# Optimization experiments

Measured on AMD Instinct MI355X. Metric: run time of the kernel, lower is better.

## Reference

```python
import jax, jax.numpy as jnp
import numpy as np

M_DIM = 32          # vec_dim m
L1 = L2 = L3 = L4 = 3
L_TOT = L1 * L2 * L3 * L4   # 81
R = 2               # rank1..rank4 window size
B_SZ = 4
D_SZ = 16           # D1 = D2 = D3 = D4


def _make_bbasis():
    # Bbasis[idx, i] = prod_k cos(2*pi*(j_k+1)/(i+2)), idx = flattened (j1,j2,j3,j4)
    i = jnp.arange(M_DIM, dtype=jnp.float32)
    def c(Lk):
        j = jnp.arange(Lk, dtype=jnp.float32)
        return jnp.cos(2.0 * jnp.pi * (j[:, None] + 1.0) / (i[None, :] + 2.0))  # [Lk, m]
    c1, c2, c3, c4 = c(L1), c(L2), c(L3), c(L4)
    Bb = (c1[:, None, None, None, :] * c2[None, :, None, None, :]
          * c3[None, None, :, None, :] * c4[None, None, None, :, :])
    return Bb.reshape(L_TOT, M_DIM)


def _window_basis_idx(n1, n2, n3, n4):
    # linear mode, drop: window top-left coords are 0..n_k-1 with step 1
    j1 = jnp.arange(n1) % L1
    j2 = jnp.arange(n2) % L2
    j3 = jnp.arange(n3) % L3
    j4 = jnp.arange(n4) % L4
    idx = (((j1[:, None, None, None] * L2 + j2[None, :, None, None]) * L3
            + j3[None, None, :, None]) * L4 + j4[None, None, None, :])
    return idx.reshape(-1)  # [n_windows]


def setup_inputs() -> dict:
    key = jax.random.key(0)
    k1, k2, k3 = jax.random.split(key, 3)
    arr_batch = jax.random.normal(k1, (B_SZ, D_SZ, D_SZ, D_SZ, D_SZ, M_DIM), dtype=jnp.float32)
    # M initialized near identity (nn.init.eye_ + perturbation so grads are non-trivial)
    M = jnp.eye(M_DIM, dtype=jnp.float32) + 0.01 * jax.random.normal(k2, (M_DIM, M_DIM), dtype=jnp.float32)
    # Acoeff ~ U(-0.1, 0.1) as in reset_parameters
    Acoeff = jax.random.uniform(k3, (M_DIM, L_TOT), dtype=jnp.float32, minval=-0.1, maxval=0.1)
    Bbasis = _make_bbasis()  # fixed buffer, computed deterministically
    return {"arr_batch": arr_batch, "M": M, "Acoeff": Acoeff, "Bbasis": Bbasis}


def reference(arr_batch, M, Acoeff, Bbasis):
    Bsz, D1, D2, D3, D4, m = arr_batch.shape
    # map every vector through M (x @ M.T); avg-pooling commutes with the linear map,
    # matching `mapped = windows @ M.T` then mean over the window
    mapped = jnp.einsum('bpqrsm,nm->bpqrsn', arr_batch, M)
    # 4D sliding window (rank=2 per dim, stride 1, 'drop' -> VALID), rank_op='avg'
    win = (1, R, R, R, R, 1)
    agg = jax.lax.reduce_window(mapped, 0.0, jax.lax.add, win, (1,) * 6, 'VALID') / float(R ** 4)
    n1, n2, n3, n4 = agg.shape[1:5]
    n_win = n1 * n2 * n3 * n4
    agg = agg.reshape(Bsz, n_win, m)            # [B, W, m]
    idx = _window_basis_idx(n1, n2, n3, n4)     # [W]
    phi = Bbasis[idx]                           # [W, m]
    # t_k = Acoeff[:, j_k] * (Bbasis[j_k, :] . agg_k); representation = mean_k t_k
    s = jnp.einsum('bwm,wm->bw', agg, phi)      # [B, W]
    t = s[:, :, None] * Acoeff.T[idx][None]     # [B, W, m]
    return t.mean(axis=1)                       # [B, m]
```

## Files before the change

kernel.cpp:

```cpp
#include <hip/hip_runtime.h>


static __device__ __forceinline__ void add4(float4& a, const float4& b) {
    a.x += b.x; a.y += b.y; a.z += b.z; a.w += b.w;
}

__global__ __launch_bounds__(128) void sdd4_prep(
    const float* __restrict__ Mmat,
    const float* __restrict__ Bbasis,
    float* __restrict__ G,
    float* __restrict__ out)
{
    __shared__ float M_lds[32 * 33];
    const int t  = threadIdx.x;
    const int bx = blockIdx.x;

    const float4* M4 = reinterpret_cast<const float4*>(Mmat);
    for (int i = t; i < 256; i += 128) {
        float4 v = M4[i];
        float* dst = &M_lds[(i >> 3) * 33 + (i & 7) * 4];
        dst[0] = v.x; dst[1] = v.y; dst[2] = v.z; dst[3] = v.w;
    }
    if (bx == 0 && t < 128) out[t] = 0.0f;
    __syncthreads();

    const int base = bx * 648;
    for (int k = 0; k < 6; ++k) {
        const int o = base + t + k * 128;
        if (o < base + 648) {
            const int jf = o >> 5, m = o & 31;
            const float4* Br = reinterpret_cast<const float4*>(Bbasis + jf * 32);
            float acc = 0.f;
            #pragma unroll
            for (int nv = 0; nv < 8; ++nv) {
                float4 bv = Br[nv];
                acc = fmaf(bv.x, M_lds[(nv * 4 + 0) * 33 + m], acc);
                acc = fmaf(bv.y, M_lds[(nv * 4 + 1) * 33 + m], acc);
                acc = fmaf(bv.z, M_lds[(nv * 4 + 2) * 33 + m], acc);
                acc = fmaf(bv.w, M_lds[(nv * 4 + 3) * 33 + m], acc);
            }
            G[o] = acc;
        }
    }
}

__global__ __launch_bounds__(256) void sdd4_main(
    const float* __restrict__ arr,
    const float* __restrict__ G,
    const float* __restrict__ Acoeff,
    float* __restrict__ out)
{
    __shared__ float4 U_lds[800];
    __shared__ float  V_lds[9 * 33];
    __shared__ float  G_lds[81 * 33];
    __shared__ __align__(16) float A_lds[32 * 81];
    __shared__ float  c_lds[40];
    __shared__ int    jf_lds[40];

    const int t  = threadIdx.x;
    const int bx = blockIdx.x;
    const int b  = bx >> 8;
    const int p  = (bx >> 4) & 15;
    const int q  = bx & 15;

    const int mv = t & 7;
    const int h  = (t >> 3) & 1;
    const int r  = t >> 4;

    const float4* A4 = reinterpret_cast<const float4*>(arr);
    const size_t tile = (size_t)((b * 16 + p) * 16 + q) * 2048;
    float4 x[8];
    #pragma unroll
    for (int i = 0; i < 8; ++i)
        x[i] = A4[tile + (size_t)((r * 16 + h * 8 + i) * 8 + mv)];

    const float4* G4 = reinterpret_cast<const float4*>(G);
    for (int i = t; i < 648; i += 256) {
        float4 v = G4[i];
        float* dst = &G_lds[(i >> 3) * 33 + (i & 7) * 4];
        dst[0] = v.x; dst[1] = v.y; dst[2] = v.z; dst[3] = v.w;
    }
    const float4* Ac4 = reinterpret_cast<const float4*>(Acoeff);
    float4* Al4 = reinterpret_cast<float4*>(A_lds);
    for (int i = t; i < 648; i += 256)
        Al4[i] = Ac4[i];

    float4 u0 = make_float4(0.f, 0.f, 0.f, 0.f), u1 = u0, u2 = u0;
    const unsigned m0 = 0x36DBu >> (h * 8);
    const unsigned m1 = 0x6DB6u >> (h * 8);
    const unsigned m2 = 0xDB6Cu >> (h * 8);
    #pragma unroll
    for (int i = 0; i < 8; ++i) {
        if ((m0 >> i) & 1) add4(u0, x[i]);
        if ((m1 >> i) & 1) add4(u1, x[i]);
        if ((m2 >> i) & 1) add4(u2, x[i]);
    }
    const int ub = (r * 2 + h) * 25;
    U_lds[ub +      mv] = u0;
    U_lds[ub +  8 + mv] = u1;
    U_lds[ub + 16 + mv] = u2;
    __syncthreads();

    if (t < 72) {
        const int j3  = t / 24;
        const int rem = t % 24;
        const int j4  = rem >> 3;
        const int mv2 = rem & 7;
        const unsigned msk = (j3 == 0) ? 0x36DBu : (j3 == 1 ? 0x6DB6u : 0xDB6Cu);
        float4 acc = make_float4(0.f, 0.f, 0.f, 0.f);
        #pragma unroll
        for (int rr = 0; rr < 16; ++rr) {
            if ((msk >> rr) & 1) {
                add4(acc, U_lds[(rr * 2 + 0) * 25 + j4 * 8 + mv2]);
                add4(acc, U_lds[(rr * 2 + 1) * 25 + j4 * 8 + mv2]);
            }
        }
        const int jj = j3 * 3 + j4;
        float* dv = &V_lds[jj * 33 + mv2 * 4];
        dv[0] = acc.x; dv[1] = acc.y; dv[2] = acc.z; dv[3] = acc.w;
    }
    __syncthreads();

    int l1_0, l1_1 = 0, n1;
    if      (p == 0)  { l1_0 = 0; n1 = 1; }
    else if (p == 15) { l1_0 = 2; n1 = 1; }
    else              { l1_0 = (p - 1) % 3; l1_1 = p % 3; n1 = 2; }
    int l2_0, l2_1 = 0, n2;
    if      (q == 0)  { l2_0 = 0; n2 = 1; }
    else if (q == 15) { l2_0 = 2; n2 = 1; }
    else              { l2_0 = (q - 1) % 3; l2_1 = q % 3; n2 = 2; }

    const int ncomb = n1 * n2 * 9;
    if (t < ncomb) {
        const int jj  = t % 9;
        const int c12 = t / 9;
        const int i1idx = (n2 == 2) ? (c12 >> 1) : c12;
        const int i2idx = (n2 == 2) ? (c12 & 1)  : 0;
        const int i1 = i1idx ? l1_1 : l1_0;
        const int i2 = i2idx ? l2_1 : l2_0;
        const int jf = (i1 * 3 + i2) * 9 + jj;
        float acc = 0.f;
        #pragma unroll
        for (int m = 0; m < 32; ++m)
            acc = fmaf(G_lds[jf * 33 + m], V_lds[jj * 33 + m], acc);
        c_lds[t]  = acc;
        jf_lds[t] = jf;
    }
    __syncthreads();

    if (t < 32) {
        float acc = 0.f;
        for (int k = 0; k < ncomb; ++k)
            acc = fmaf(A_lds[t * 81 + jf_lds[k]], c_lds[k], acc);
        atomicAdd(&out[b * 32 + t], acc * (1.0f / 810000.0f));
    }
}

extern "C" void kernel_launch(void* const* d_in, const int* in_sizes, int n_in,
                              void* d_out, int out_size, void* d_ws, size_t ws_size,
                              hipStream_t stream) {
    const float* arr    = (const float*)d_in[0];
    const float* Mmat   = (const float*)d_in[1];
    const float* Acoeff = (const float*)d_in[2];
    const float* Bbasis = (const float*)d_in[3];
    float* G = (float*)d_ws;

    sdd4_prep<<<dim3(4),    dim3(128), 0, stream>>>(Mmat, Bbasis, G, (float*)d_out);
    sdd4_main<<<dim3(1024), dim3(256), 0, stream>>>(arr, G, Acoeff, (float*)d_out);
}
```

Measured before the change: 88.22 us.

## Fold M projection into main kernel and replace atomics with a reduce kernel

Drops the prep kernel that precomputed G = Bbasis·M. Each main block now applies M to its 9 window sums (Y = M·V) and then dots Y with Bbasis rows read from global memory. Acoeff is also read directly from global instead of being staged in LDS, which removes the large G and A shared-memory staging and shrinks LDS use. The per-batch atomicAdd is replaced by per-block partial sums written to workspace and then summed by a single-block reduce kernel. This trades a little extra per-block arithmetic for less LDS traffic, fewer prep-to-main dependencies and no atomic contention, at the cost of a serial final reduction.

```diff
diff --git a/kernel.cpp b/kernel.cpp
--- a/kernel.cpp
+++ b/kernel.cpp
@@ -5,57 +5,19 @@
     a.x += b.x; a.y += b.y; a.z += b.z; a.w += b.w;
 }
 
-__global__ __launch_bounds__(128) void sdd4_prep(
+__global__ __launch_bounds__(256) void sdd4_main(
+    const float* __restrict__ arr,
     const float* __restrict__ Mmat,
     const float* __restrict__ Bbasis,
-    float* __restrict__ G,
-    float* __restrict__ out)
-{
-    __shared__ float M_lds[32 * 33];
-    const int t  = threadIdx.x;
-    const int bx = blockIdx.x;
-
-    const float4* M4 = reinterpret_cast<const float4*>(Mmat);
-    for (int i = t; i < 256; i += 128) {
-        float4 v = M4[i];
-        float* dst = &M_lds[(i >> 3) * 33 + (i & 7) * 4];
-        dst[0] = v.x; dst[1] = v.y; dst[2] = v.z; dst[3] = v.w;
-    }
-    if (bx == 0 && t < 128) out[t] = 0.0f;
-    __syncthreads();
-
-    const int base = bx * 648;
-    for (int k = 0; k < 6; ++k) {
-        const int o = base + t + k * 128;
-        if (o < base + 648) {
-            const int jf = o >> 5, m = o & 31;
-            const float4* Br = reinterpret_cast<const float4*>(Bbasis + jf * 32);
-            float acc = 0.f;
-            #pragma unroll
-            for (int nv = 0; nv < 8; ++nv) {
-                float4 bv = Br[nv];
-                acc = fmaf(bv.x, M_lds[(nv * 4 + 0) * 33 + m], acc);
-                acc = fmaf(bv.y, M_lds[(nv * 4 + 1) * 33 + m], acc);
-                acc = fmaf(bv.z, M_lds[(nv * 4 + 2) * 33 + m], acc);
-                acc = fmaf(bv.w, M_lds[(nv * 4 + 3) * 33 + m], acc);
-            }
-            G[o] = acc;
-        }
-    }
-}
-
-__global__ __launch_bounds__(256) void sdd4_main(
-    const float* __restrict__ arr,
-    const float* __restrict__ G,
     const float* __restrict__ Acoeff,
-    float* __restrict__ out)
+    float* __restrict__ ws)
 {
     __shared__ float4 U_lds[800];
     __shared__ float  V_lds[9 * 33];
-    __shared__ float  G_lds[81 * 33];
-    __shared__ __align__(16) float A_lds[32 * 81];
-    __shared__ float  c_lds[40];
-    __shared__ int    jf_lds[40];
+    __shared__ float  M_lds[32 * 33];
+    __shared__ float  Y_lds[9 * 33];
+    __shared__ float  c_lds[36];
+    __shared__ int    jf_lds[36];
 
     const int t  = threadIdx.x;
     const int bx = blockIdx.x;
@@ -74,16 +36,12 @@
     for (int i = 0; i < 8; ++i)
         x[i] = A4[tile + (size_t)((r * 16 + h * 8 + i) * 8 + mv)];
 
-    const float4* G4 = reinterpret_cast<const float4*>(G);
-    for (int i = t; i < 648; i += 256) {
-        float4 v = G4[i];
-        float* dst = &G_lds[(i >> 3) * 33 + (i & 7) * 4];
+    {
+        const float4* M4 = reinterpret_cast<const float4*>(Mmat);
+        float4 v = M4[t];
+        float* dst = &M_lds[(t >> 3) * 33 + (t & 7) * 4];
         dst[0] = v.x; dst[1] = v.y; dst[2] = v.z; dst[3] = v.w;
     }
-    const float4* Ac4 = reinterpret_cast<const float4*>(Acoeff);
-    float4* Al4 = reinterpret_cast<float4*>(A_lds);
-    for (int i = t; i < 648; i += 256)
-        Al4[i] = Ac4[i];
 
     float4 u0 = make_float4(0.f, 0.f, 0.f, 0.f), u1 = u0, u2 = u0;
     const unsigned m0 = 0x36DBu >> (h * 8);
@@ -121,6 +79,17 @@
     }
     __syncthreads();
 
+    for (int o = t; o < 288; o += 256) {
+        const int jj = o >> 5;
+        const int n  = o & 31;
+        float acc = 0.f;
+        #pragma unroll
+        for (int m = 0; m < 32; ++m)
+            acc = fmaf(M_lds[n * 33 + m], V_lds[jj * 33 + m], acc);
+        Y_lds[jj * 33 + n] = acc;
+    }
+    __syncthreads();
+
     int l1_0, l1_1 = 0, n1;
     if      (p == 0)  { l1_0 = 0; n1 = 1; }
     else if (p == 15) { l1_0 = 2; n1 = 1; }
@@ -139,10 +108,11 @@
         const int i1 = i1idx ? l1_1 : l1_0;
         const int i2 = i2idx ? l2_1 : l2_0;
         const int jf = (i1 * 3 + i2) * 9 + jj;
+        const float* Br = Bbasis + jf * 32;
         float acc = 0.f;
         #pragma unroll
-        for (int m = 0; m < 32; ++m)
-            acc = fmaf(G_lds[jf * 33 + m], V_lds[jj * 33 + m], acc);
+        for (int n = 0; n < 32; ++n)
+            acc = fmaf(Br[n], Y_lds[jj * 33 + n], acc);
         c_lds[t]  = acc;
         jf_lds[t] = jf;
     }
@@ -151,9 +121,23 @@
     if (t < 32) {
         float acc = 0.f;
         for (int k = 0; k < ncomb; ++k)
-            acc = fmaf(A_lds[t * 81 + jf_lds[k]], c_lds[k], acc);
-        atomicAdd(&out[b * 32 + t], acc * (1.0f / 810000.0f));
+            acc = fmaf(Acoeff[t * 81 + jf_lds[k]], c_lds[k], acc);
+        ws[bx * 32 + t] = acc;
     }
+}
+
+__global__ __launch_bounds__(128) void sdd4_reduce(
+    const float* __restrict__ ws,
+    float* __restrict__ out)
+{
+    const int t = threadIdx.x;
+    const int b = t >> 5;
+    const int n = t & 31;
+    float acc = 0.f;
+    #pragma unroll 8
+    for (int pq = 0; pq < 256; ++pq)
+        acc += ws[(b * 256 + pq) * 32 + n];
+    out[t] = acc * (1.0f / 810000.0f);
 }
 
 extern "C" void kernel_launch(void* const* d_in, const int* in_sizes, int n_in,
@@ -163,8 +147,8 @@
     const float* Mmat   = (const float*)d_in[1];
     const float* Acoeff = (const float*)d_in[2];
     const float* Bbasis = (const float*)d_in[3];
-    float* G = (float*)d_ws;
+    float* ws = (float*)d_ws;
 
-    sdd4_prep<<<dim3(4),    dim3(128), 0, stream>>>(Mmat, Bbasis, G, (float*)d_out);
-    sdd4_main<<<dim3(1024), dim3(256), 0, stream>>>(arr, G, Acoeff, (float*)d_out);
+    sdd4_main<<<dim3(1024), dim3(256), 0, stream>>>(arr, Mmat, Bbasis, Acoeff, ws);
+    sdd4_reduce<<<dim3(1), dim3(128), 0, stream>>>(ws, (float*)d_out);
 }
```

Measured after the change: 90.97 us. 3.1% more time.
